# Performance work log

Hardware: AMD Instinct MI355X
Metric: run time of the kernel (lower is better)

Reference implementation:

```python
import jax, jax.numpy as jnp
import numpy as np

BATCH, NODE, DIM = 4, 2048, 128
EPS = 1e-5


def _bn(x, gamma, beta):
    # BatchNorm1d in training mode: biased batch stats over rows, per-feature.
    mu = jnp.mean(x, axis=0)
    var = jnp.var(x, axis=0)
    return (x - mu) * jax.lax.rsqrt(var + EPS) * gamma + beta


def setup_inputs() -> dict:
    key = jax.random.key(0)
    ks = jax.random.split(key, 8)
    N = BATCH * NODE
    # Scale L like a normalized graph operator so activations stay sane.
    L = jax.random.normal(ks[0], (N, N), dtype=jnp.float32) / np.sqrt(N)
    inputs = jax.random.normal(ks[1], (BATCH, NODE, DIM), dtype=jnp.float32)
    mask = jnp.zeros((BATCH, NODE, 1), dtype=bool)  # unused in forward
    lim = 1.0 / np.sqrt(2 * DIM)
    fc0_w = jax.random.uniform(ks[2], (DIM, 2 * DIM), jnp.float32, -lim, lim)
    fc0_b = jax.random.uniform(ks[3], (DIM,), jnp.float32, -lim, lim)
    fc1_w = jax.random.uniform(ks[4], (DIM, 2 * DIM), jnp.float32, -lim, lim)
    fc1_b = jax.random.uniform(ks[5], (DIM,), jnp.float32, -lim, lim)
    bn0_gamma = jnp.ones((2 * DIM,), jnp.float32)
    bn0_beta = jnp.zeros((2 * DIM,), jnp.float32)
    bn1_gamma = jnp.ones((2 * DIM,), jnp.float32)
    bn1_beta = jnp.zeros((2 * DIM,), jnp.float32)
    return dict(L=L, mask=mask, inputs=inputs,
                bn0_gamma=bn0_gamma, bn0_beta=bn0_beta, fc0_w=fc0_w, fc0_b=fc0_b,
                bn1_gamma=bn1_gamma, bn1_beta=bn1_beta, fc1_w=fc1_w, fc1_b=fc1_b)


def reference(L, mask, inputs, bn0_gamma, bn0_beta, fc0_w, fc0_b,
              bn1_gamma, bn1_beta, fc1_w, fc1_b):
    b, n, d = inputs.shape

    def block(x, gamma, beta, w, bias):
        # x: (b, n, d). Laplacian propagation over flattened batch*node dim.
        xf = x.reshape(-1, d)                      # (b*n, d)
        Lx = (L @ xf).reshape(b, n, d)
        h = jnp.concatenate([x, Lx], axis=2).reshape(-1, 2 * d)
        h = _bn(h, gamma, beta)                    # pre-BN
        h = h @ w.T + bias                         # Linear(2d -> d)
        return h.reshape(b, n, d)

    x = jax.nn.elu(inputs)
    x = block(x, bn0_gamma, bn0_beta, fc0_w, fc0_b)
    x = jax.nn.elu(x)
    x = block(x, bn1_gamma, bn1_beta, fc1_w, fc1_b)
    return x + inputs
```

## Files before the change

### kernel.cpp

```cpp
#include <hip/hip_runtime.h>
#include <math.h>

#define NROWS 8192
#define DIM   128
#define FEAT  256
#define BK    128
#define NT    (NROWS / BK)

typedef __attribute__((ext_vector_type(8))) __bf16 bf16x8;
typedef __attribute__((ext_vector_type(8))) unsigned short u16x8;
typedef __attribute__((ext_vector_type(4))) unsigned short u16x4;
typedef __attribute__((ext_vector_type(4))) float f32x4;

__device__ __forceinline__ float bf2f(unsigned short h) {
  return __uint_as_float(((unsigned)h) << 16);
}
__device__ __forceinline__ unsigned short f2bf(float f) {
  unsigned u = __float_as_uint(f);
  return (unsigned short)((u + 0x7fff + ((u >> 16) & 1)) >> 16);
}
__device__ __forceinline__ void async16(const void* g, void* l) {
  __builtin_amdgcn_global_load_lds(
      (const __attribute__((address_space(1))) void*)g,
      (__attribute__((address_space(3))) void*)l, 16, 0, 0);
}
__device__ __forceinline__ f32x4 mfma16(bf16x8 a, bf16x8 b, f32x4 c) {
  return __builtin_amdgcn_mfma_f32_16x16x32_bf16(a, b, c, 0, 0, 0);
}
__device__ __forceinline__ float ldp(const void* p, int i, int is32) {
  return is32 ? ((const float*)p)[i] : bf2f(((const unsigned short*)p)[i]);
}

__global__ void detect_kernel(const unsigned short* __restrict__ L,
                              int* __restrict__ flag,
                              float* __restrict__ stats)
{
  for (int i = threadIdx.x; i < 1024; i += 256) stats[i] = 0.f;
  __shared__ int cnt;
  if (threadIdx.x == 0) cnt = 0;
  __syncthreads();
  int c = 0;
  for (int i = 0; i < 16; i++) {
    unsigned short s = L[2 * (threadIdx.x + 256 * i)];
    int e = (s >> 7) & 0xFF;
    if (e >= 192) c++;
  }
  atomicAdd(&cnt, c);
  __syncthreads();
  if (threadIdx.x == 0) *flag = (cnt > 16) ? 1 : 0;
}

__global__ __launch_bounds__(256) void trans_kernel(
    const void* __restrict__ src, unsigned short* __restrict__ xT,
    unsigned short* __restrict__ x0, unsigned short* __restrict__ inpc,
    float* __restrict__ stats, const int* __restrict__ flag)
{
  __shared__ __align__(16) unsigned short T[128 * 136];
  const int tid = threadIdx.x;
  const int r0 = blockIdx.x * 128;
  const int is32 = *flag;
  #pragma unroll
  for (int i = 0; i < 8; i++) {
    const int c = tid + 256 * i;
    const int rr = c >> 4, cg = c & 15;
    const size_t gidx = (size_t)(r0 + rr) * DIM + cg * 8;
    u16x8 v;
    if (is32) {
      const float* s = (const float*)src + gidx;
      f32x4 a = *(const f32x4*)s, b = *(const f32x4*)(s + 4);
      #pragma unroll
      for (int e = 0; e < 4; e++) { v[e] = f2bf(a[e]); v[e + 4] = f2bf(b[e]); }
    } else {
      v = *(const u16x8*)((const unsigned short*)src + gidx);
    }
    *(u16x8*)(inpc + gidx) = v;
    #pragma unroll
    for (int e = 0; e < 8; e++) {
      float f = bf2f(v[e]);
      f = f > 0.f ? f : expm1f(f);
      v[e] = f2bf(f);
    }
    *(u16x8*)(x0 + gidx) = v;
    *(u16x8*)(T + rr * 136 + cg * 8) = v;
  }
  __syncthreads();
  #pragma unroll
  for (int i = 0; i < 8; i++) {
    const int c = tid + 256 * i;
    const int n = c >> 4, mg = c & 15;
    u16x8 v;
    float s = 0.f, q = 0.f;
    #pragma unroll
    for (int e = 0; e < 8; e++) {
      unsigned short h = T[(mg * 8 + e) * 136 + n];
      v[e] = h;
      float f = bf2f(h);
      s += f; q += f * f;
    }
    *(u16x8*)(xT + (size_t)n * NROWS + r0 + mg * 8) = v;
    #pragma unroll
    for (int off = 1; off < 16; off <<= 1) {
      s += __shfl_xor(s, off, 16);
      q += __shfl_xor(q, off, 16);
    }
    if ((tid & 15) == 0) {
      atomicAdd(&stats[n], s);
      atomicAdd(&stats[256 + n], q);
    }
  }
}

template <int IS32>
__device__ __forceinline__ void gemm1_body(
    const void* __restrict__ Lraw, const unsigned short* __restrict__ xT,
    unsigned short* __restrict__ Lxb, float* __restrict__ stats,
    unsigned short* __restrict__ AsBase, unsigned short* __restrict__ BsBase)
{
  const int tid  = threadIdx.x;
  const int lane = tid & 63;
  const int wave = tid >> 6;
  const int wm = wave >> 2, wn = wave & 3;
  const int ln = lane & 15, quad = lane >> 4;
  const int m0 = blockIdx.x * 32;

  const int arow = tid >> 4, ap = tid & 15;
  const int akg = (ap & 8) | ((ap & 7) ^ (arow & 7));
  const float*          Lf = (const float*)Lraw;
  const unsigned short* Lh = (const unsigned short*)Lraw;
  const size_t Abase = (size_t)(m0 + arow) * NROWS + akg * 8;

  int brow[4], bkg[4];
  #pragma unroll
  for (int i = 0; i < 4; i++) {
    const int c = tid + (i << 9);
    brow[i] = c >> 4;
    const int p = c & 15;
    bkg[i] = (p & 8) | ((p & 7) ^ (brow[i] & 7));
  }

  unsigned short* a0 = AsBase;
  unsigned short* a1 = AsBase + 32 * 128;
  unsigned short* a2 = AsBase + 2 * 32 * 128;
  unsigned short* c0 = BsBase;
  unsigned short* c1 = BsBase + 128 * 128;
  unsigned short* c2 = BsBase + 2 * 128 * 128;

  f32x4 acc[2];
  acc[0] = (f32x4){0.f, 0.f, 0.f, 0.f};
  acc[1] = (f32x4){0.f, 0.f, 0.f, 0.f};

  auto issueB = [&](int kt, unsigned short* Bbuf) {
    const size_t koff = (size_t)kt * BK;
    #pragma unroll
    for (int i = 0; i < 4; i++) {
      const int c = tid + (i << 9);
      async16(xT + (size_t)brow[i] * NROWS + koff + bkg[i] * 8, Bbuf + c * 8);
    }
  };
  auto loadA = [&](int kt, f32x4& r0, f32x4& r1) {
    const float* s = Lf + Abase + (size_t)kt * BK;
    r0 = *(const f32x4*)s;
    r1 = *(const f32x4*)(s + 4);
  };
  auto issueA16 = [&](int kt, unsigned short* Abuf) {
    async16(Lh + Abase + (size_t)kt * BK, Abuf + arow * 128 + ap * 8);
  };
  auto writeA = [&](const f32x4& r0, const f32x4& r1, unsigned short* Abuf) {
    u16x8 o;
    #pragma unroll
    for (int e = 0; e < 4; e++) { o[e] = f2bf(r0[e]); o[e + 4] = f2bf(r1[e]); }
    *(u16x8*)(Abuf + arow * 128 + ap * 8) = o;
  };
  auto compute = [&](const unsigned short* Abuf, const unsigned short* Bbuf) {
    const int arf = wm * 16 + ln;
    const int brf = wn * 32 + ln;
    #pragma unroll
    for (int ks = 0; ks < 4; ks++) {
      const int kga = ks * 4 + quad;
      bf16x8 af = *(const bf16x8*)(Abuf + arf * 128 +
                     ((kga & 8) | ((kga & 7) ^ (arf & 7))) * 8);
      #pragma unroll
      for (int j = 0; j < 2; j++) {
        const int rb = brf + j * 16;
        bf16x8 bf = *(const bf16x8*)(Bbuf + rb * 128 +
                       ((kga & 8) | ((kga & 7) ^ (rb & 7))) * 8);
        acc[j] = mfma16(af, bf, acc[j]);
      }
    }
  };
  auto waitbar = [&]() {
    if (IS32) asm volatile("s_waitcnt vmcnt(6) lgkmcnt(0)" ::: "memory");
    else      asm volatile("s_waitcnt vmcnt(5) lgkmcnt(0)" ::: "memory");
    __builtin_amdgcn_s_barrier();
  };

  f32x4 e0, e1, o0, o1;

  issueB(0, c0);
  if (IS32) loadA(0, e0, e1); else issueA16(0, a0);
  issueB(1, c1);
  if (IS32) loadA(1, o0, o1); else issueA16(1, a1);
  if (IS32) writeA(e0, e1, a0);
  waitbar();

  for (int p = 0; p < 31; ++p) {
    const int t = 2 * p;
    issueB(t + 2, c2);
    if (IS32) loadA(t + 2, e0, e1); else issueA16(t + 2, a2);
    compute(a0, c0);
    if (IS32) writeA(o0, o1, a1);
    waitbar();
    issueB(t + 3, c0);
    if (IS32) loadA(t + 3, o0, o1); else issueA16(t + 3, a0);
    compute(a1, c1);
    if (IS32) writeA(e0, e1, a2);
    waitbar();
    unsigned short* tB = c2; c2 = c1; c1 = c0; c0 = tB;
    unsigned short* tA = a2; a2 = a1; a1 = a0; a0 = tA;
  }

  compute(a0, c0);
  if (IS32) writeA(o0, o1, a1);
  __syncthreads();
  compute(a1, c1);
  __syncthreads();

  float* E = (float*)AsBase;
  #pragma unroll
  for (int j = 0; j < 2; j++) {
    const int col = wn * 32 + j * 16 + ln;
    #pragma unroll
    for (int r = 0; r < 4; r++)
      E[(wm * 16 + quad * 4 + r) * 128 + col] = acc[j][r];
  }
  __syncthreads();
  {
    const int row = tid >> 4, cc0 = (tid & 15) * 8;
    u16x8 o;
    #pragma unroll
    for (int e = 0; e < 8; e++) o[e] = f2bf(E[row * 128 + cc0 + e]);
    *(u16x8*)(Lxb + (size_t)(m0 + row) * DIM + cc0) = o;
  }
  if (tid < 128) {
    float s = 0.f, q = 0.f;
    #pragma unroll
    for (int r = 0; r < 32; r++) {
      const float v = E[r * 128 + tid];
      s += v; q += v * v;
    }
    atomicAdd(&stats[128 + tid], s);
    atomicAdd(&stats[384 + tid], q);
  }
}

__global__ __launch_bounds__(512) void gemm1_fused(
    const void* __restrict__ Lraw, const unsigned short* __restrict__ xT,
    unsigned short* __restrict__ Lxb, float* __restrict__ stats,
    const int* __restrict__ flag)
{
  __shared__ __align__(16) unsigned short As[3 * 32 * 128];
  __shared__ __align__(16) unsigned short Bs[3 * 128 * 128];
  if (*flag) gemm1_body<1>(Lraw, xT, Lxb, stats, As, Bs);
  else       gemm1_body<0>(Lraw, xT, Lxb, stats, As, Bs);
}

__global__ void prep_kernel(const float* __restrict__ stats,
                            const void* __restrict__ gamma,
                            const void* __restrict__ beta,
                            const void* __restrict__ w,
                            const void* __restrict__ bias,
                            unsigned short* __restrict__ weff,
                            float* __restrict__ beff,
                            const int* __restrict__ flag)
{
  const int is32 = *flag;
  const int k = blockIdx.x;
  const int j = threadIdx.x;
  const float inv = 1.f / 8192.f;
  float mu = stats[j] * inv;
  float var = fmaxf(stats[256 + j] * inv - mu * mu, 0.f);
  float s = ldp(gamma, j, is32) * rsqrtf(var + 1e-5f);
  float wv = ldp(w, k * FEAT + j, is32);
  weff[(size_t)k * FEAT + j] = f2bf(wv * s);
  float term = (ldp(beta, j, is32) - mu * s) * wv;
  __shared__ float red[256];
  red[j] = term;
  __syncthreads();
  for (int off = 128; off > 0; off >>= 1) {
    if (j < off) red[j] += red[j + off];
    __syncthreads();
  }
  if (j == 0) beff[k] = ldp(bias, k, is32) + red[0];
}

__global__ __launch_bounds__(256) void gemm2_fc(
    const unsigned short* __restrict__ xb,
    const unsigned short* __restrict__ Lxb,
    const unsigned short* __restrict__ weff,
    const float* __restrict__ beff,
    const unsigned short* __restrict__ resid,
    void* __restrict__ outv,
    unsigned short* __restrict__ xTout,
    float* __restrict__ statsOut,
    int mode, const int* __restrict__ flag)
{
  __shared__ __align__(16) unsigned short As[32 * 264];
  const int is32 = *flag;
  const int tid = threadIdx.x;
  const int lane = tid & 63, wave = tid >> 6;
  const int m0 = blockIdx.x * 32;

  #pragma unroll
  for (int i = 0; i < 4; i++) {
    const int c = tid + 256 * i;
    const int mr = c >> 5, ch = c & 31;
    const unsigned short* src =
        (ch < 16) ? (xb  + (size_t)(m0 + mr) * DIM + ch * 8)
                  : (Lxb + (size_t)(m0 + mr) * DIM + (ch - 16) * 8);
    *(u16x8*)(As + mr * 264 + ch * 8) = *(const u16x8*)src;
  }
  __syncthreads();

  const int ln = lane & 15, quad = lane >> 4;
  const int nq = wave * 32;
  f32x4 acc[2][2];
  #pragma unroll
  for (int i = 0; i < 2; i++)
    #pragma unroll
    for (int j = 0; j < 2; j++)
      acc[i][j] = (f32x4){0.f, 0.f, 0.f, 0.f};

  #pragma unroll
  for (int ks = 0; ks < 8; ks++) {
    bf16x8 af[2], bfr[2];
    #pragma unroll
    for (int i = 0; i < 2; i++)
      af[i] = *(const bf16x8*)(As + (i * 16 + ln) * 264 + ks * 32 + quad * 8);
    #pragma unroll
    for (int j = 0; j < 2; j++)
      bfr[j] = *(const bf16x8*)(weff + (size_t)(nq + j * 16 + ln) * FEAT +
                                ks * 32 + quad * 8);
    #pragma unroll
    for (int i = 0; i < 2; i++)
      #pragma unroll
      for (int j = 0; j < 2; j++)
        acc[i][j] = mfma16(af[i], bfr[j], acc[i][j]);
  }

  #pragma unroll
  for (int j = 0; j < 2; j++) {
    const int gn = nq + j * 16 + ln;
    const float bb = beff[gn];
    float s = 0.f, q = 0.f;
    #pragma unroll
    for (int i = 0; i < 2; i++) {
      u16x4 pk;
      #pragma unroll
      for (int r = 0; r < 4; r++) {
        const int gm = m0 + i * 16 + quad * 4 + r;
        float v = acc[i][j][r] + bb;
        const size_t idx = (size_t)gm * DIM + gn;
        if (mode == 0) {
          v = v > 0.f ? v : expm1f(v);
          const unsigned short h = f2bf(v);
          ((unsigned short*)outv)[idx] = h;
          pk[r] = h;
          const float hv = bf2f(h);
          s += hv; q += hv * hv;
        } else {
          v += bf2f(resid[idx]);
          if (is32) ((float*)outv)[idx] = v;
          else      ((unsigned short*)outv)[idx] = f2bf(v);
        }
      }
      if (mode == 0)
        *(u16x4*)(xTout + (size_t)gn * NROWS + m0 + i * 16 + quad * 4) = pk;
    }
    if (mode == 0) {
      s += __shfl_xor(s, 16); q += __shfl_xor(q, 16);
      s += __shfl_xor(s, 32); q += __shfl_xor(q, 32);
      if (quad == 0) {
        atomicAdd(&statsOut[gn], s);
        atomicAdd(&statsOut[256 + gn], q);
      }
    }
  }
}

extern "C" void kernel_launch(void* const* d_in, const int* in_sizes, int n_in,
                              void* d_out, int out_size, void* d_ws, size_t ws_size,
                              hipStream_t stream) {
  const void* Lm   = d_in[0];
  const void* inp  = d_in[2];
  const void* bn0g = d_in[3];
  const void* bn0b = d_in[4];
  const void* fc0w = d_in[5];
  const void* fc0b = d_in[6];
  const void* bn1g = d_in[7];
  const void* bn1b = d_in[8];
  const void* fc1w = d_in[9];
  const void* fc1b = d_in[10];

  char* ws = (char*)d_ws;
  unsigned short* xT   = (unsigned short*)(ws);
  unsigned short* x0   = (unsigned short*)(ws + (2ull << 20));
  unsigned short* Lxb  = (unsigned short*)(ws + (4ull << 20));
  unsigned short* x1   = (unsigned short*)(ws + (6ull << 20));
  unsigned short* inpc = (unsigned short*)(ws + (8ull << 20));
  float*          stats= (float*)         (ws + (10ull << 20));
  int*            flag = (int*)           (ws + (10ull << 20) + 8192);
  float*          beff = (float*)         (ws + (10ull << 20) + 12288);
  unsigned short* weff = (unsigned short*)(ws + (10ull << 20) + 16384);

  detect_kernel<<<1, 256, 0, stream>>>((const unsigned short*)Lm, flag, stats);

  trans_kernel<<<64, 256, 0, stream>>>(inp, xT, x0, inpc, stats, flag);
  gemm1_fused<<<256, 512, 0, stream>>>(Lm, xT, Lxb, stats, flag);
  prep_kernel<<<128, 256, 0, stream>>>(stats, bn0g, bn0b, fc0w, fc0b,
                                       weff, beff, flag);
  gemm2_fc<<<256, 256, 0, stream>>>(x0, Lxb, weff, beff, nullptr, x1,
                                    xT, stats + 512, 0, flag);

  gemm1_fused<<<256, 512, 0, stream>>>(Lm, xT, Lxb, stats + 512, flag);
  prep_kernel<<<128, 256, 0, stream>>>(stats + 512, bn1g, bn1b, fc1w, fc1b,
                                       weff, beff, flag);
  gemm2_fc<<<256, 256, 0, stream>>>(x1, Lxb, weff, beff, inpc, d_out,
                                    nullptr, nullptr, 1, flag);
}
```

Before: 184.9 us.

## Fold BN prep into gemm2, drop detect kernel, use 32x32 MFMA split-K in gemm1

Removes the detect and prep kernels. Dtype detection moves into trans_kernel, and the weights are converted to bf16 once there. gemm2 now reduces per-block partial stats and applies the BN scale and shift to its A tile on load, replacing the pre-folded weights. Stat atomics are swapped for per-block partial writes. gemm1 switches to 32x32x16 MFMA with the two wave halves splitting K and summing through LDS. This cuts launch count and atomics, but every gemm2 block now redundantly reduces up to 256 partials plus a bias dot product.

```diff
diff --git a/kernel.cpp b/kernel.cpp
--- a/kernel.cpp
+++ b/kernel.cpp
@@ -11,6 +11,7 @@
 typedef __attribute__((ext_vector_type(8))) unsigned short u16x8;
 typedef __attribute__((ext_vector_type(4))) unsigned short u16x4;
 typedef __attribute__((ext_vector_type(4))) float f32x4;
+typedef __attribute__((ext_vector_type(16))) float f32x16;
 
 __device__ __forceinline__ float bf2f(unsigned short h) {
   return __uint_as_float(((unsigned)h) << 16);
@@ -27,38 +28,50 @@
 __device__ __forceinline__ f32x4 mfma16(bf16x8 a, bf16x8 b, f32x4 c) {
   return __builtin_amdgcn_mfma_f32_16x16x32_bf16(a, b, c, 0, 0, 0);
 }
+__device__ __forceinline__ f32x16 mfma32(bf16x8 a, bf16x8 b, f32x16 c) {
+  return __builtin_amdgcn_mfma_f32_32x32x16_bf16(a, b, c, 0, 0, 0);
+}
 __device__ __forceinline__ float ldp(const void* p, int i, int is32) {
   return is32 ? ((const float*)p)[i] : bf2f(((const unsigned short*)p)[i]);
-}
-
-__global__ void detect_kernel(const unsigned short* __restrict__ L,
-                              int* __restrict__ flag,
-                              float* __restrict__ stats)
-{
-  for (int i = threadIdx.x; i < 1024; i += 256) stats[i] = 0.f;
-  __shared__ int cnt;
-  if (threadIdx.x == 0) cnt = 0;
-  __syncthreads();
-  int c = 0;
-  for (int i = 0; i < 16; i++) {
-    unsigned short s = L[2 * (threadIdx.x + 256 * i)];
-    int e = (s >> 7) & 0xFF;
-    if (e >= 192) c++;
-  }
-  atomicAdd(&cnt, c);
-  __syncthreads();
-  if (threadIdx.x == 0) *flag = (cnt > 16) ? 1 : 0;
 }
 
 __global__ __launch_bounds__(256) void trans_kernel(
     const void* __restrict__ src, unsigned short* __restrict__ xT,
     unsigned short* __restrict__ x0, unsigned short* __restrict__ inpc,
-    float* __restrict__ stats, const int* __restrict__ flag)
+    float* __restrict__ TP, int* __restrict__ flag,
+    const void* __restrict__ w0raw, const void* __restrict__ w1raw,
+    unsigned short* __restrict__ wb)
 {
   __shared__ __align__(16) unsigned short T[128 * 136];
+  __shared__ int cnt;
   const int tid = threadIdx.x;
   const int r0 = blockIdx.x * 128;
-  const int is32 = *flag;
+  if (tid == 0) cnt = 0;
+  __syncthreads();
+  {
+    const unsigned short* u = (const unsigned short*)src;
+    int c = 0;
+    #pragma unroll
+    for (int i = 0; i < 16; i++) {
+      int e = (u[tid * 16 + i] >> 7) & 0xFF;
+      if (e >= 192) c++;
+    }
+    atomicAdd(&cnt, c);
+  }
+  __syncthreads();
+  const int is32 = (cnt > 16);
+  if (tid == 0 && blockIdx.x == 0) *flag = is32;
+
+  if (blockIdx.x < 8) {
+    const int base = blockIdx.x * 8192;
+    for (int i = tid; i < 8192; i += 256) {
+      const int g = base + i;
+      const float v = (g < 32768) ? ldp(w0raw, g, is32)
+                                  : ldp(w1raw, g - 32768, is32);
+      wb[g] = f2bf(v);
+    }
+  }
+
   #pragma unroll
   for (int i = 0; i < 8; i++) {
     const int c = tid + 256 * i;
@@ -104,8 +117,8 @@
       q += __shfl_xor(q, off, 16);
     }
     if ((tid & 15) == 0) {
-      atomicAdd(&stats[n], s);
-      atomicAdd(&stats[256 + n], q);
+      TP[blockIdx.x * 256 + n] = s;
+      TP[blockIdx.x * 256 + 128 + n] = q;
     }
   }
 }
@@ -113,14 +126,13 @@
 template <int IS32>
 __device__ __forceinline__ void gemm1_body(
     const void* __restrict__ Lraw, const unsigned short* __restrict__ xT,
-    unsigned short* __restrict__ Lxb, float* __restrict__ stats,
+    unsigned short* __restrict__ Lxb, float* __restrict__ GP,
     unsigned short* __restrict__ AsBase, unsigned short* __restrict__ BsBase)
 {
   const int tid  = threadIdx.x;
   const int lane = tid & 63;
   const int wave = tid >> 6;
-  const int wm = wave >> 2, wn = wave & 3;
-  const int ln = lane & 15, quad = lane >> 4;
+  const int wn = wave & 3, kh = wave >> 2;
   const int m0 = blockIdx.x * 32;
 
   const int arow = tid >> 4, ap = tid & 15;
@@ -145,9 +157,9 @@
   unsigned short* c1 = BsBase + 128 * 128;
   unsigned short* c2 = BsBase + 2 * 128 * 128;
 
-  f32x4 acc[2];
-  acc[0] = (f32x4){0.f, 0.f, 0.f, 0.f};
-  acc[1] = (f32x4){0.f, 0.f, 0.f, 0.f};
+  f32x16 acc;
+  #pragma unroll
+  for (int r = 0; r < 16; r++) acc[r] = 0.f;
 
   auto issueB = [&](int kt, unsigned short* Bbuf) {
     const size_t koff = (size_t)kt * BK;
@@ -171,21 +183,18 @@
     for (int e = 0; e < 4; e++) { o[e] = f2bf(r0[e]); o[e + 4] = f2bf(r1[e]); }
     *(u16x8*)(Abuf + arow * 128 + ap * 8) = o;
   };
+  const int fr = lane & 31;
+  const int ksel = lane >> 5;
+  const int brf = wn * 32 + fr;
   auto compute = [&](const unsigned short* Abuf, const unsigned short* Bbuf) {
-    const int arf = wm * 16 + ln;
-    const int brf = wn * 32 + ln;
-    #pragma unroll
-    for (int ks = 0; ks < 4; ks++) {
-      const int kga = ks * 4 + quad;
-      bf16x8 af = *(const bf16x8*)(Abuf + arf * 128 +
-                     ((kga & 8) | ((kga & 7) ^ (arf & 7))) * 8);
-      #pragma unroll
-      for (int j = 0; j < 2; j++) {
-        const int rb = brf + j * 16;
-        bf16x8 bf = *(const bf16x8*)(Bbuf + rb * 128 +
-                       ((kga & 8) | ((kga & 7) ^ (rb & 7))) * 8);
-        acc[j] = mfma16(af, bf, acc[j]);
-      }
+    #pragma unroll
+    for (int km = 0; km < 4; km++) {
+      const int kg = kh * 8 + km * 2 + ksel;
+      bf16x8 af = *(const bf16x8*)(Abuf + fr * 128 +
+                     ((kg & 8) | ((kg & 7) ^ (fr & 7))) * 8);
+      bf16x8 bf = *(const bf16x8*)(Bbuf + brf * 128 +
+                     ((kg & 8) | ((kg & 7) ^ (brf & 7))) * 8);
+      acc = mfma32(af, bf, acc);
     }
   };
   auto waitbar = [&]() {
@@ -226,12 +235,18 @@
   __syncthreads();
 
   float* E = (float*)AsBase;
-  #pragma unroll
-  for (int j = 0; j < 2; j++) {
-    const int col = wn * 32 + j * 16 + ln;
-    #pragma unroll
-    for (int r = 0; r < 4; r++)
-      E[(wm * 16 + quad * 4 + r) * 128 + col] = acc[j][r];
+  const int ecol = wn * 32 + fr;
+  const int rb4 = 4 * ksel;
+  if (kh == 0) {
+    #pragma unroll
+    for (int r = 0; r < 16; r++)
+      E[((r & 3) + 8 * (r >> 2) + rb4) * 128 + ecol] = acc[r];
+  }
+  __syncthreads();
+  if (kh == 1) {
+    #pragma unroll
+    for (int r = 0; r < 16; r++)
+      E[((r & 3) + 8 * (r >> 2) + rb4) * 128 + ecol] += acc[r];
   }
   __syncthreads();
   {
@@ -248,67 +263,77 @@
       const float v = E[r * 128 + tid];
       s += v; q += v * v;
     }
-    atomicAdd(&stats[128 + tid], s);
-    atomicAdd(&stats[384 + tid], q);
+    GP[blockIdx.x * 256 + tid] = s;
+    GP[blockIdx.x * 256 + 128 + tid] = q;
   }
 }
 
 __global__ __launch_bounds__(512) void gemm1_fused(
     const void* __restrict__ Lraw, const unsigned short* __restrict__ xT,
-    unsigned short* __restrict__ Lxb, float* __restrict__ stats,
+    unsigned short* __restrict__ Lxb, float* __restrict__ GP,
     const int* __restrict__ flag)
 {
   __shared__ __align__(16) unsigned short As[3 * 32 * 128];
   __shared__ __align__(16) unsigned short Bs[3 * 128 * 128];
-  if (*flag) gemm1_body<1>(Lraw, xT, Lxb, stats, As, Bs);
-  else       gemm1_body<0>(Lraw, xT, Lxb, stats, As, Bs);
-}
-
-__global__ void prep_kernel(const float* __restrict__ stats,
-                            const void* __restrict__ gamma,
-                            const void* __restrict__ beta,
-                            const void* __restrict__ w,
-                            const void* __restrict__ bias,
-                            unsigned short* __restrict__ weff,
-                            float* __restrict__ beff,
-                            const int* __restrict__ flag)
-{
-  const int is32 = *flag;
-  const int k = blockIdx.x;
-  const int j = threadIdx.x;
-  const float inv = 1.f / 8192.f;
-  float mu = stats[j] * inv;
-  float var = fmaxf(stats[256 + j] * inv - mu * mu, 0.f);
-  float s = ldp(gamma, j, is32) * rsqrtf(var + 1e-5f);
-  float wv = ldp(w, k * FEAT + j, is32);
-  weff[(size_t)k * FEAT + j] = f2bf(wv * s);
-  float term = (ldp(beta, j, is32) - mu * s) * wv;
-  __shared__ float red[256];
-  red[j] = term;
-  __syncthreads();
-  for (int off = 128; off > 0; off >>= 1) {
-    if (j < off) red[j] += red[j + off];
-    __syncthreads();
-  }
-  if (j == 0) beff[k] = ldp(bias, k, is32) + red[0];
+  if (*flag) gemm1_body<1>(Lraw, xT, Lxb, GP, As, Bs);
+  else       gemm1_body<0>(Lraw, xT, Lxb, GP, As, Bs);
 }
 
 __global__ __launch_bounds__(256) void gemm2_fc(
     const unsigned short* __restrict__ xb,
     const unsigned short* __restrict__ Lxb,
-    const unsigned short* __restrict__ weff,
-    const float* __restrict__ beff,
+    const unsigned short* __restrict__ wb,
+    const void* __restrict__ gamma, const void* __restrict__ beta,
+    const void* __restrict__ bias,
+    const float* __restrict__ Px, int nPx,
+    const float* __restrict__ Plx,
     const unsigned short* __restrict__ resid,
     void* __restrict__ outv,
     unsigned short* __restrict__ xTout,
-    float* __restrict__ statsOut,
+    float* __restrict__ XPout,
     int mode, const int* __restrict__ flag)
 {
   __shared__ __align__(16) unsigned short As[32 * 264];
+  __shared__ float sS[256], sMS[256], bred[256], bv[128];
   const int is32 = *flag;
   const int tid = threadIdx.x;
   const int lane = tid & 63, wave = tid >> 6;
   const int m0 = blockIdx.x * 32;
+
+  {
+    const int j = tid;
+    float s = 0.f, q = 0.f;
+    if (j < 128) {
+      for (int b = 0; b < nPx; b++) {
+        s += Px[b * 256 + j]; q += Px[b * 256 + 128 + j];
+      }
+    } else {
+      const int jj = j - 128;
+      for (int b = 0; b < 256; b++) {
+        s += Plx[b * 256 + jj]; q += Plx[b * 256 + 128 + jj];
+      }
+    }
+    const float inv = 1.f / 8192.f;
+    const float mu = s * inv;
+    const float var = fmaxf(q * inv - mu * mu, 0.f);
+    const float sj = ldp(gamma, j, is32) * rsqrtf(var + 1e-5f);
+    sS[j] = sj;
+    sMS[j] = mu * sj;
+  }
+  {
+    const int k = tid & 127, half = tid >> 7;
+    float a = 0.f;
+    for (int jj = 0; jj < 128; jj += 8) {
+      u16x8 wv = *(const u16x8*)(wb + k * 256 + half * 128 + jj);
+      #pragma unroll
+      for (int e = 0; e < 8; e++)
+        a += ldp(beta, half * 128 + jj + e, is32) * bf2f(wv[e]);
+    }
+    bred[tid] = a;
+  }
+  __syncthreads();
+  if (tid < 128)
+    bv[tid] = ldp(bias, tid, is32) + bred[tid] + bred[tid + 128];
 
   #pragma unroll
   for (int i = 0; i < 4; i++) {
@@ -317,7 +342,14 @@
     const unsigned short* src =
         (ch < 16) ? (xb  + (size_t)(m0 + mr) * DIM + ch * 8)
                   : (Lxb + (size_t)(m0 + mr) * DIM + (ch - 16) * 8);
-    *(u16x8*)(As + mr * 264 + ch * 8) = *(const u16x8*)src;
+    u16x8 v = *(const u16x8*)src;
+    const int j0 = ch * 8;
+    #pragma unroll
+    for (int e = 0; e < 8; e++) {
+      const float f = bf2f(v[e]);
+      v[e] = f2bf(f * sS[j0 + e] - sMS[j0 + e]);
+    }
+    *(u16x8*)(As + mr * 264 + ch * 8) = v;
   }
   __syncthreads();
 
@@ -338,7 +370,7 @@
       af[i] = *(const bf16x8*)(As + (i * 16 + ln) * 264 + ks * 32 + quad * 8);
     #pragma unroll
     for (int j = 0; j < 2; j++)
-      bfr[j] = *(const bf16x8*)(weff + (size_t)(nq + j * 16 + ln) * FEAT +
+      bfr[j] = *(const bf16x8*)(wb + (size_t)(nq + j * 16 + ln) * FEAT +
                                 ks * 32 + quad * 8);
     #pragma unroll
     for (int i = 0; i < 2; i++)
@@ -350,7 +382,7 @@
   #pragma unroll
   for (int j = 0; j < 2; j++) {
     const int gn = nq + j * 16 + ln;
-    const float bb = beff[gn];
+    const float bb = bv[gn];
     float s = 0.f, q = 0.f;
     #pragma unroll
     for (int i = 0; i < 2; i++) {
@@ -380,8 +412,8 @@
       s += __shfl_xor(s, 16); q += __shfl_xor(q, 16);
       s += __shfl_xor(s, 32); q += __shfl_xor(q, 32);
       if (quad == 0) {
-        atomicAdd(&statsOut[gn], s);
-        atomicAdd(&statsOut[256 + gn], q);
+        XPout[blockIdx.x * 256 + gn] = s;
+        XPout[blockIdx.x * 256 + 128 + gn] = q;
       }
     }
   }
@@ -407,23 +439,22 @@
   unsigned short* Lxb  = (unsigned short*)(ws + (4ull << 20));
   unsigned short* x1   = (unsigned short*)(ws + (6ull << 20));
   unsigned short* inpc = (unsigned short*)(ws + (8ull << 20));
-  float*          stats= (float*)         (ws + (10ull << 20));
-  int*            flag = (int*)           (ws + (10ull << 20) + 8192);
-  float*          beff = (float*)         (ws + (10ull << 20) + 12288);
-  unsigned short* weff = (unsigned short*)(ws + (10ull << 20) + 16384);
-
-  detect_kernel<<<1, 256, 0, stream>>>((const unsigned short*)Lm, flag, stats);
-
-  trans_kernel<<<64, 256, 0, stream>>>(inp, xT, x0, inpc, stats, flag);
-  gemm1_fused<<<256, 512, 0, stream>>>(Lm, xT, Lxb, stats, flag);
-  prep_kernel<<<128, 256, 0, stream>>>(stats, bn0g, bn0b, fc0w, fc0b,
-                                       weff, beff, flag);
-  gemm2_fc<<<256, 256, 0, stream>>>(x0, Lxb, weff, beff, nullptr, x1,
-                                    xT, stats + 512, 0, flag);
-
-  gemm1_fused<<<256, 512, 0, stream>>>(Lm, xT, Lxb, stats + 512, flag);
-  prep_kernel<<<128, 256, 0, stream>>>(stats + 512, bn1g, bn1b, fc1w, fc1b,
-                                       weff, beff, flag);
-  gemm2_fc<<<256, 256, 0, stream>>>(x1, Lxb, weff, beff, inpc, d_out,
+  float*          TP0  = (float*)(ws + (10ull << 20));
+  float*          GPa  = (float*)(ws + (10ull << 20) + (256u << 10));
+  float*          XP   = (float*)(ws + (10ull << 20) + (512u << 10));
+  float*          GPb  = (float*)(ws + (10ull << 20) + (768u << 10));
+  unsigned short* wb   = (unsigned short*)(ws + (11ull << 20));
+  int*            flag = (int*)(ws + (11ull << 20) + (512u << 10));
+
+  trans_kernel<<<64, 256, 0, stream>>>(inp, xT, x0, inpc, TP0, flag,
+                                       fc0w, fc1w, wb);
+  gemm1_fused<<<256, 512, 0, stream>>>(Lm, xT, Lxb, GPa, flag);
+  gemm2_fc<<<256, 256, 0, stream>>>(x0, Lxb, wb, bn0g, bn0b, fc0b,
+                                    TP0, 64, GPa, nullptr, x1,
+                                    xT, XP, 0, flag);
+
+  gemm1_fused<<<256, 512, 0, stream>>>(Lm, xT, Lxb, GPb, flag);
+  gemm2_fc<<<256, 256, 0, stream>>>(x1, Lxb, wb + 32768, bn1g, bn1b, fc1b,
+                                    XP, 256, GPb, inpc, d_out,
                                     nullptr, nullptr, 1, flag);
 }
```

Result: slower. 275.7 us (+49.1%).

## Fold BatchNorm into GEMM2 prologue and drop prep kernels

Applied to the files above, without the earlier changes.

Removes the two prep_kernel launches that built scaled weights and an effective bias. The raw fc weights are now converted to bf16 once inside trans_kernel. Each gemm2 block recomputes the per-feature BN scale and shift from the stats, applies them to the activations as it loads them into LDS, and computes the beta·W bias term itself. This also adds s_setprio around the MFMA loop in gemm1. The cost is redundant per-block stats and bias work plus a small extra rounding step on the activations.

```diff
diff --git a/kernel.cpp b/kernel.cpp
--- a/kernel.cpp
+++ b/kernel.cpp
@@ -53,12 +53,25 @@
 __global__ __launch_bounds__(256) void trans_kernel(
     const void* __restrict__ src, unsigned short* __restrict__ xT,
     unsigned short* __restrict__ x0, unsigned short* __restrict__ inpc,
-    float* __restrict__ stats, const int* __restrict__ flag)
+    float* __restrict__ stats, const int* __restrict__ flag,
+    const void* __restrict__ w0raw, const void* __restrict__ w1raw,
+    unsigned short* __restrict__ wb)
 {
   __shared__ __align__(16) unsigned short T[128 * 136];
   const int tid = threadIdx.x;
   const int r0 = blockIdx.x * 128;
   const int is32 = *flag;
+
+  if (blockIdx.x < 8) {
+    const int base = blockIdx.x * 8192;
+    for (int i = tid; i < 8192; i += 256) {
+      const int g = base + i;
+      const float v = (g < 32768) ? ldp(w0raw, g, is32)
+                                  : ldp(w1raw, g - 32768, is32);
+      wb[g] = f2bf(v);
+    }
+  }
+
   #pragma unroll
   for (int i = 0; i < 8; i++) {
     const int c = tid + 256 * i;
@@ -174,6 +187,7 @@
   auto compute = [&](const unsigned short* Abuf, const unsigned short* Bbuf) {
     const int arf = wm * 16 + ln;
     const int brf = wn * 32 + ln;
+    __builtin_amdgcn_s_setprio(1);
     #pragma unroll
     for (int ks = 0; ks < 4; ks++) {
       const int kga = ks * 4 + quad;
@@ -187,6 +201,7 @@
         acc[j] = mfma16(af, bf, acc[j]);
       }
     }
+    __builtin_amdgcn_s_setprio(0);
   };
   auto waitbar = [&]() {
     if (IS32) asm volatile("s_waitcnt vmcnt(6) lgkmcnt(0)" ::: "memory");
@@ -264,40 +279,13 @@
   else       gemm1_body<0>(Lraw, xT, Lxb, stats, As, Bs);
 }
 
-__global__ void prep_kernel(const float* __restrict__ stats,
-                            const void* __restrict__ gamma,
-                            const void* __restrict__ beta,
-                            const void* __restrict__ w,
-                            const void* __restrict__ bias,
-                            unsigned short* __restrict__ weff,
-                            float* __restrict__ beff,
-                            const int* __restrict__ flag)
-{
-  const int is32 = *flag;
-  const int k = blockIdx.x;
-  const int j = threadIdx.x;
-  const float inv = 1.f / 8192.f;
-  float mu = stats[j] * inv;
-  float var = fmaxf(stats[256 + j] * inv - mu * mu, 0.f);
-  float s = ldp(gamma, j, is32) * rsqrtf(var + 1e-5f);
-  float wv = ldp(w, k * FEAT + j, is32);
-  weff[(size_t)k * FEAT + j] = f2bf(wv * s);
-  float term = (ldp(beta, j, is32) - mu * s) * wv;
-  __shared__ float red[256];
-  red[j] = term;
-  __syncthreads();
-  for (int off = 128; off > 0; off >>= 1) {
-    if (j < off) red[j] += red[j + off];
-    __syncthreads();
-  }
-  if (j == 0) beff[k] = ldp(bias, k, is32) + red[0];
-}
-
 __global__ __launch_bounds__(256) void gemm2_fc(
     const unsigned short* __restrict__ xb,
     const unsigned short* __restrict__ Lxb,
-    const unsigned short* __restrict__ weff,
-    const float* __restrict__ beff,
+    const unsigned short* __restrict__ wb,
+    const void* __restrict__ gamma, const void* __restrict__ beta,
+    const void* __restrict__ bias,
+    const float* __restrict__ stats,
     const unsigned short* __restrict__ resid,
     void* __restrict__ outv,
     unsigned short* __restrict__ xTout,
@@ -305,10 +293,36 @@
     int mode, const int* __restrict__ flag)
 {
   __shared__ __align__(16) unsigned short As[32 * 264];
+  __shared__ float sS[256], sMS[256], bred[256], bv[128];
   const int is32 = *flag;
   const int tid = threadIdx.x;
   const int lane = tid & 63, wave = tid >> 6;
   const int m0 = blockIdx.x * 32;
+
+  {
+    const int j = tid;
+    const float inv = 1.f / 8192.f;
+    const float mu = stats[j] * inv;
+    const float var = fmaxf(stats[256 + j] * inv - mu * mu, 0.f);
+    const float sj = ldp(gamma, j, is32) * rsqrtf(var + 1e-5f);
+    sS[j] = sj;
+    sMS[j] = mu * sj;
+  }
+  {
+    const int k = tid & 127, half = tid >> 7;
+    float a = 0.f;
+    #pragma unroll
+    for (int jj = 0; jj < 128; jj += 8) {
+      u16x8 wv = *(const u16x8*)(wb + k * 256 + half * 128 + jj);
+      #pragma unroll
+      for (int e = 0; e < 8; e++)
+        a += ldp(beta, half * 128 + jj + e, is32) * bf2f(wv[e]);
+    }
+    bred[tid] = a;
+  }
+  __syncthreads();
+  if (tid < 128)
+    bv[tid] = ldp(bias, tid, is32) + bred[tid] + bred[tid + 128];
 
   #pragma unroll
   for (int i = 0; i < 4; i++) {
@@ -317,7 +331,14 @@
     const unsigned short* src =
         (ch < 16) ? (xb  + (size_t)(m0 + mr) * DIM + ch * 8)
                   : (Lxb + (size_t)(m0 + mr) * DIM + (ch - 16) * 8);
-    *(u16x8*)(As + mr * 264 + ch * 8) = *(const u16x8*)src;
+    u16x8 v = *(const u16x8*)src;
+    const int j0 = ch * 8;
+    #pragma unroll
+    for (int e = 0; e < 8; e++) {
+      const float f = bf2f(v[e]);
+      v[e] = f2bf(f * sS[j0 + e] - sMS[j0 + e]);
+    }
+    *(u16x8*)(As + mr * 264 + ch * 8) = v;
   }
   __syncthreads();
 
@@ -338,7 +359,7 @@
       af[i] = *(const bf16x8*)(As + (i * 16 + ln) * 264 + ks * 32 + quad * 8);
     #pragma unroll
     for (int j = 0; j < 2; j++)
-      bfr[j] = *(const bf16x8*)(weff + (size_t)(nq + j * 16 + ln) * FEAT +
+      bfr[j] = *(const bf16x8*)(wb + (size_t)(nq + j * 16 + ln) * FEAT +
                                 ks * 32 + quad * 8);
     #pragma unroll
     for (int i = 0; i < 2; i++)
@@ -350,7 +371,7 @@
   #pragma unroll
   for (int j = 0; j < 2; j++) {
     const int gn = nq + j * 16 + ln;
-    const float bb = beff[gn];
+    const float bb = bv[gn];
     float s = 0.f, q = 0.f;
     #pragma unroll
     for (int i = 0; i < 2; i++) {
@@ -409,21 +430,19 @@
   unsigned short* inpc = (unsigned short*)(ws + (8ull << 20));
   float*          stats= (float*)         (ws + (10ull << 20));
   int*            flag = (int*)           (ws + (10ull << 20) + 8192);
-  float*          beff = (float*)         (ws + (10ull << 20) + 12288);
-  unsigned short* weff = (unsigned short*)(ws + (10ull << 20) + 16384);
+  unsigned short* wb   = (unsigned short*)(ws + (10ull << 20) + 16384);
 
   detect_kernel<<<1, 256, 0, stream>>>((const unsigned short*)Lm, flag, stats);
 
-  trans_kernel<<<64, 256, 0, stream>>>(inp, xT, x0, inpc, stats, flag);
+  trans_kernel<<<64, 256, 0, stream>>>(inp, xT, x0, inpc, stats, flag,
+                                       fc0w, fc1w, wb);
   gemm1_fused<<<256, 512, 0, stream>>>(Lm, xT, Lxb, stats, flag);
-  prep_kernel<<<128, 256, 0, stream>>>(stats, bn0g, bn0b, fc0w, fc0b,
-                                       weff, beff, flag);
-  gemm2_fc<<<256, 256, 0, stream>>>(x0, Lxb, weff, beff, nullptr, x1,
+  gemm2_fc<<<256, 256, 0, stream>>>(x0, Lxb, wb, bn0g, bn0b, fc0b,
+                                    stats, nullptr, x1,
                                     xT, stats + 512, 0, flag);
 
   gemm1_fused<<<256, 512, 0, stream>>>(Lm, xT, Lxb, stats + 512, flag);
-  prep_kernel<<<128, 256, 0, stream>>>(stats + 512, bn1g, bn1b, fc1w, fc1b,
-                                       weff, beff, flag);
-  gemm2_fc<<<256, 256, 0, stream>>>(x1, Lxb, weff, beff, inpc, d_out,
+  gemm2_fc<<<256, 256, 0, stream>>>(x1, Lxb, wb + 32768, bn1g, bn1b, fc1b,
+                                    stats + 512, inpc, d_out,
                                     nullptr, nullptr, 1, flag);
 }
```

Result: slower. 207.2 us (+12.1%).

## Split K across wave halves in Lx GEMM with LDS reduction

Applied to the files above, without the earlier changes.

Reassigns the 8 waves of the L@x GEMM so each wave group covers half of every 128-wide K tile and the full 32-row output, computing a 2x2 grid of MFMA tiles per wave instead of 1x2. Each A and B fragment loaded from LDS is now reused across two MFMAs, which cuts LDS reads per MFMA. The two K-halves' partial sums are combined through the LDS epilogue buffer, at the cost of an extra barrier and a read-modify-write pass. Accumulator register usage doubles.

```diff
diff --git a/kernel.cpp b/kernel.cpp
--- a/kernel.cpp
+++ b/kernel.cpp
@@ -119,7 +119,7 @@
   const int tid  = threadIdx.x;
   const int lane = tid & 63;
   const int wave = tid >> 6;
-  const int wm = wave >> 2, wn = wave & 3;
+  const int kh = wave >> 2, wq = wave & 3;
   const int ln = lane & 15, quad = lane >> 4;
   const int m0 = blockIdx.x * 32;
 
@@ -145,9 +145,12 @@
   unsigned short* c1 = BsBase + 128 * 128;
   unsigned short* c2 = BsBase + 2 * 128 * 128;
 
-  f32x4 acc[2];
-  acc[0] = (f32x4){0.f, 0.f, 0.f, 0.f};
-  acc[1] = (f32x4){0.f, 0.f, 0.f, 0.f};
+  f32x4 acc[2][2];
+  #pragma unroll
+  for (int i = 0; i < 2; i++)
+    #pragma unroll
+    for (int j = 0; j < 2; j++)
+      acc[i][j] = (f32x4){0.f, 0.f, 0.f, 0.f};
 
   auto issueB = [&](int kt, unsigned short* Bbuf) {
     const size_t koff = (size_t)kt * BK;
@@ -172,20 +175,18 @@
     *(u16x8*)(Abuf + arow * 128 + ap * 8) = o;
   };
   auto compute = [&](const unsigned short* Abuf, const unsigned short* Bbuf) {
-    const int arf = wm * 16 + ln;
-    const int brf = wn * 32 + ln;
-    #pragma unroll
-    for (int ks = 0; ks < 4; ks++) {
-      const int kga = ks * 4 + quad;
-      bf16x8 af = *(const bf16x8*)(Abuf + arf * 128 +
-                     ((kga & 8) | ((kga & 7) ^ (arf & 7))) * 8);
-      #pragma unroll
-      for (int j = 0; j < 2; j++) {
-        const int rb = brf + j * 16;
-        bf16x8 bf = *(const bf16x8*)(Bbuf + rb * 128 +
-                       ((kga & 8) | ((kga & 7) ^ (rb & 7))) * 8);
-        acc[j] = mfma16(af, bf, acc[j]);
-      }
+    #pragma unroll
+    for (int s = 0; s < 2; s++) {
+      const int kga = kh * 8 + s * 4 + quad;
+      const int sw8 = ((kga & 8) | ((kga & 7) ^ (ln & 7))) * 8;
+      bf16x8 af0 = *(const bf16x8*)(Abuf + ln * 128 + sw8);
+      bf16x8 af1 = *(const bf16x8*)(Abuf + (16 + ln) * 128 + sw8);
+      bf16x8 bf0 = *(const bf16x8*)(Bbuf + (wq * 32 + ln) * 128 + sw8);
+      bf16x8 bf1 = *(const bf16x8*)(Bbuf + (wq * 32 + 16 + ln) * 128 + sw8);
+      acc[0][0] = mfma16(af0, bf0, acc[0][0]);
+      acc[0][1] = mfma16(af0, bf1, acc[0][1]);
+      acc[1][0] = mfma16(af1, bf0, acc[1][0]);
+      acc[1][1] = mfma16(af1, bf1, acc[1][1]);
     }
   };
   auto waitbar = [&]() {
@@ -227,11 +228,25 @@
 
   float* E = (float*)AsBase;
   #pragma unroll
-  for (int j = 0; j < 2; j++) {
-    const int col = wn * 32 + j * 16 + ln;
-    #pragma unroll
-    for (int r = 0; r < 4; r++)
-      E[(wm * 16 + quad * 4 + r) * 128 + col] = acc[j][r];
+  for (int i = 0; i < 2; i++)
+    #pragma unroll
+    for (int j = 0; j < 2; j++)
+      if (kh == 0) {
+        #pragma unroll
+        for (int r = 0; r < 4; r++)
+          E[(i * 16 + quad * 4 + r) * 128 + wq * 32 + j * 16 + ln] =
+              acc[i][j][r];
+      }
+  __syncthreads();
+  if (kh == 1) {
+    #pragma unroll
+    for (int i = 0; i < 2; i++)
+      #pragma unroll
+      for (int j = 0; j < 2; j++)
+        #pragma unroll
+        for (int r = 0; r < 4; r++)
+          E[(i * 16 + quad * 4 + r) * 128 + wq * 32 + j * 16 + ln] +=
+              acc[i][j][r];
   }
   __syncthreads();
   {
```

Result: faster. 178.8 us (-3.3%).
